# Kernel tuning notes

Measured on AMD Instinct MI355X. Metric: run time of the kernel, lower is better.

Reference implementation:

```python
import jax, jax.numpy as jnp
import numpy as np

FIR = (1.0, 3.0, 3.0, 1.0)
FACTOR = 2
GAIN = 1.0


def _fir_kernel_2d():
    # _setup_kernel: 1D -> outer product, normalize, then scale by gain*factor^2
    k = np.asarray(FIR, dtype=np.float32)
    k = np.outer(k, k)
    k /= k.sum()
    return k * (GAIN * FACTOR ** 2)  # [4, 4]


def setup_inputs() -> dict:
    key = jax.random.key(0)
    kx, kw = jax.random.split(key)
    x = jax.random.normal(kx, (4, 256, 64, 64), dtype=jnp.float32)
    # DDPM variance-scaling init ~ U(-sqrt(3*var), sqrt(3*var)); plain scaled normal is fine for a numeric baseline
    w = jax.random.normal(kw, (256, 256, 3, 3), dtype=jnp.float32) * 0.02  # [outC, inC, 3, 3]
    return {"x": x, "w": w}


def reference(x, w):
    # Fused upsample(+FIR) conv: torch does conv_transpose2d(x, flip(w).permute(in,out), stride=2)
    # which is exactly a correlation of the stride-2 zero-dilated input with the ORIGINAL OIHW weight.
    N, C, H, W = x.shape
    outC, inC, kh, kw_ = w.shape
    h = jax.lax.conv_general_dilated(
        x, w,
        window_strides=(1, 1),
        padding=((kh - 1, kh - 1), (kw_ - 1, kw_ - 1)),
        lhs_dilation=(FACTOR, FACTOR),
        dimension_numbers=("NCHW", "OIHW", "NCHW"),
    )  # [N, outC, 2H+1, 2W+1]

    k = jnp.asarray(_fir_kernel_2d())  # [4,4]
    p = k.shape[0] - FACTOR - (kw_ - 1)          # = 0
    pad0 = (p + 1) // 2 + FACTOR - 1             # = 1
    pad1 = p // 2 + 1                            # = 1
    # upfirdn2d with up=1, down=1, pad=(pad0,pad1): pad then TRUE convolution (flipped kernel),
    # applied depthwise per channel.
    kflip = k[::-1, ::-1]
    kern = jnp.tile(kflip[None, None, :, :], (outC, 1, 1, 1))  # [outC, 1, 4, 4]
    out = jax.lax.conv_general_dilated(
        h, kern,
        window_strides=(1, 1),
        padding=((pad0, pad1), (pad0, pad1)),
        dimension_numbers=("NCHW", "OIHW", "NCHW"),
        feature_group_count=outC,
    )  # [N, outC, 2H, 2W]
    return out
```

## Files before the change

### kernel.cpp

```cpp
#include <hip/hip_runtime.h>
#include <hip/hip_bf16.h>


typedef short short2v __attribute__((ext_vector_type(2)));
typedef short bf16x8 __attribute__((ext_vector_type(8)));
typedef short short4v __attribute__((ext_vector_type(4)));
typedef float f32x2v __attribute__((ext_vector_type(2)));
typedef float f32x16 __attribute__((ext_vector_type(16)));
typedef float f32x4v __attribute__((ext_vector_type(4)));

static __device__ __forceinline__ short f2bf(float f) {
  __hip_bfloat16 h = __float2bfloat16(f);
  union { __hip_bfloat16 h; short s; } u; u.h = h;
  return u.s;
}
static __device__ __forceinline__ float bf2f(short s) {
  union { unsigned u; float f; } v; v.u = ((unsigned)(unsigned short)s) << 16;
  return v.f;
}

#define AS_SZ 18432
#define XS_BASE 36864
#define XS_SZ 8640
#define XS_STRIDE 48

__global__ __launch_bounds__(512, 2)
void fir_up_v15(const float* __restrict__ x, const float* __restrict__ w,
                float* __restrict__ out) {
  __shared__ __align__(16) char smem[54144];

  const int bid = blockIdx.x;
  const int wg = (bid & 7) * 64 + (bid >> 3);
  const int octile = wg >> 7;
  const int n = (wg >> 5) & 3;
  const int sp = wg & 31;
  const int atile = sp >> 2;
  const int btile = sp & 3;
  const int A0 = atile * 8, B0 = btile * 16;

  const int tid = threadIdx.x;
  const int wid = tid >> 6;
  const int lane = tid & 63;
  const int l31 = lane & 31, q = lane >> 5;

  const int COLSt[4]  = {17, 18, 17, 18};
  const int CELLSt[4] = {153, 162, 170, 180};
  const int NKt[4]    = {4, 2, 2, 1};
  const int KQt[4][4] = {{0,2,6,8},{1,7,7,7},{3,5,5,5},{4,4,4,4}};
  const int DYt[4][4] = {{0,0,1,1},{0,1,1,1},{0,0,0,0},{0,0,0,0}};
  const int DXt[4][4] = {{0,1,0,1},{0,0,0,0},{0,1,1,1},{0,0,0,0}};
  const unsigned long long PLbits =
      (0x34ULL) | (0x34ULL << 6) | (0x34ULL << 12) | (0x38ULL << 18) |
      (0x38ULL << 24) | (0x38ULL << 30) | (0x15ULL << 36) | (0x2AULL << 42);
  const unsigned FG0 = 0u | 1u<<3 | 2u<<6 | 3u<<9 | 4u<<12 | 5u<<15 | 3u<<18 | 3u<<21;
  const unsigned FG1 = 0u | 1u<<3 | 2u<<6 | 0u<<9 | 1u<<12 | 2u<<15 | 4u<<18 | 4u<<21;
  const unsigned FG2 = 0u | 1u<<3 | 2u<<6 | 3u<<9 | 4u<<12 | 5u<<15 | 5u<<18 | 5u<<21;

  int nkS[3], validS[3], hbaseS[3];
  int kqS[3][4], cellxS[3][4];
#pragma unroll
  for (int slot = 0; slot < 3; ++slot) {
    const int p = (int)((PLbits >> ((wid * 3 + slot) * 2)) & 3ULL);
    const unsigned fgw = slot == 0 ? FG0 : (slot == 1 ? FG1 : FG2);
    const int fg = (int)((fgw >> (3 * wid)) & 7u);
    const int cellraw = fg * 32 + l31;
    const int valid = cellraw < CELLSt[p];
    const int cell = valid ? cellraw : 0;
    const int cols = COLSt[p];
    const int r = cell / cols;
    const int c = cell - r * cols;
    nkS[slot] = NKt[p];
    validS[slot] = valid;
    hbaseS[slot] = p * 6400 + r * 20 + c;
#pragma unroll
    for (int s = 0; s < 4; ++s) {
      kqS[slot][s] = KQt[p][s];
      cellxS[slot][s] = (r + DYt[p][s]) * 18 + (c + DXt[p][s]);
    }
  }

  f32x16 acc[3][2];
#pragma unroll
  for (int slot = 0; slot < 3; ++slot)
#pragma unroll
    for (int mf = 0; mf < 2; ++mf)
#pragma unroll
      for (int e = 0; e < 16; ++e) acc[slot][mf][e] = 0.f;

  const int ocA = tid >> 3, icp = tid & 7;
  const float* wA = w + (size_t)(octile * 64 + ocA) * 2304 + icp * 18;
  int uic_[2], urow_[2], uf4g_[2], ugh_[2], ugw0_[2], uwb0_[2];
  bool uact_[2], urowok_[2], ual_[2], uint_[2];
#pragma unroll
  for (int t = 0; t < 2; ++t) {
    const int u = tid + t * 512;
    uact_[t] = u < 960;
    const int uu = uact_[t] ? u : 0;
    uic_[t] = uu / 60;
    const int rem = uu - uic_[t] * 60;
    urow_[t] = rem / 6;
    uf4g_[t] = rem - urow_[t] * 6;
    ugh_[t] = A0 - 1 + urow_[t];
    urowok_[t] = (ugh_[t] >= 0) & (ugh_[t] < 64);
    ugw0_[t] = B0 - 4 + 4 * uf4g_[t];
    ual_[t] = (ugw0_[t] >= 0) & (ugw0_[t] <= 60);
    uint_[t] = (uf4g_[t] >= 1) & (uf4g_[t] <= 4);
    uwb0_[t] = (urow_[t] * 18 + (4 * uf4g_[t] - 3)) * XS_STRIDE + uic_[t] * 2;
  }

  {
    char* xsw = smem + XS_BASE;
#pragma unroll
    for (int t = 0; t < 2; ++t) {
      if (uact_[t]) {
        float v[4] = {0.f, 0.f, 0.f, 0.f};
        if (urowok_[t]) {
          const float* base = x + (((size_t)(n * 256 + uic_[t])) * 64 + ugh_[t]) * 64;
          if (ual_[t]) {
            const f32x4v fv = *(const f32x4v*)(base + ugw0_[t]);
#pragma unroll
            for (int e = 0; e < 4; ++e) v[e] = fv[e];
          } else {
#pragma unroll
            for (int e = 0; e < 4; ++e) {
              const int gw = ugw0_[t] + e;
              v[e] = (gw >= 0 && gw < 64) ? base[gw] : 0.f;
            }
          }
        }
        if (uint_[t]) {
#pragma unroll
          for (int e = 0; e < 4; ++e)
            *(short*)(xsw + uwb0_[t] + e * XS_STRIDE) = f2bf(v[e]);
        } else {
#pragma unroll
          for (int e = 0; e < 4; ++e) {
            const int ww = 4 * uf4g_[t] + e - 3;
            if (ww >= 0 && ww < 18)
              *(short*)(xsw + (urow_[t] * 18 + ww) * XS_STRIDE + uic_[t] * 2) = f2bf(v[e]);
          }
        }
      }
    }
    float f18[18];
#pragma unroll
    for (int j = 0; j < 9; ++j)
      *(f32x2v*)&f18[2 * j] = *(const f32x2v*)(wA + 2 * j);
#pragma unroll
    for (int kq = 0; kq < 9; ++kq) {
      short2v pk;
      pk[0] = f2bf(f18[kq]);
      pk[1] = f2bf(f18[kq + 9]);
      *(short2v*)(smem + kq * 2048 + ocA * 32 + icp * 4) = pk;
    }
  }
  __syncthreads();

  for (int cc = 0; cc < 16; ++cc) {
    char* Asr = smem + (cc & 1) * AS_SZ;
    char* xsr = smem + XS_BASE + (cc & 1) * XS_SZ;
    char* Asw = smem + ((cc + 1) & 1) * AS_SZ;
    char* xsw = smem + XS_BASE + ((cc + 1) & 1) * XS_SZ;
    const bool have = cc < 15;

    float xv[2][4];
#pragma unroll
    for (int t = 0; t < 2; ++t) {
#pragma unroll
      for (int e = 0; e < 4; ++e) xv[t][e] = 0.f;
      if (have && uact_[t] && urowok_[t]) {
        const float* base =
            x + (((size_t)(n * 256 + (cc + 1) * 16 + uic_[t])) * 64 + ugh_[t]) * 64;
        if (ual_[t]) {
          const f32x4v fv = *(const f32x4v*)(base + ugw0_[t]);
#pragma unroll
          for (int e = 0; e < 4; ++e) xv[t][e] = fv[e];
        } else {
#pragma unroll
          for (int e = 0; e < 4; ++e) {
            const int gw = ugw0_[t] + e;
            xv[t][e] = (gw >= 0 && gw < 64) ? base[gw] : 0.f;
          }
        }
      }
    }

    __builtin_amdgcn_s_setprio(1);
#pragma unroll
    for (int slot = 0; slot < 3; ++slot) {
#pragma unroll
      for (int s = 0; s < 4; ++s) {
        if (s < nkS[slot]) {
          const int kq = kqS[slot][s];
          const bf16x8 B  = *(const bf16x8*)(xsr + cellxS[slot][s] * XS_STRIDE + q * 16);
          const bf16x8 Aa = *(const bf16x8*)(Asr + kq * 2048 + l31 * 32 + q * 16);
          const bf16x8 Ab = *(const bf16x8*)(Asr + kq * 2048 + 1024 + l31 * 32 + q * 16);
          acc[slot][0] = __builtin_amdgcn_mfma_f32_32x32x16_bf16(Aa, B, acc[slot][0], 0, 0, 0);
          acc[slot][1] = __builtin_amdgcn_mfma_f32_32x32x16_bf16(Ab, B, acc[slot][1], 0, 0, 0);
        }
      }
    }
    __builtin_amdgcn_s_setprio(0);

    if (have) {
#pragma unroll
      for (int t = 0; t < 2; ++t) {
        if (uact_[t]) {
          if (uint_[t]) {
#pragma unroll
            for (int e = 0; e < 4; ++e)
              *(short*)(xsw + uwb0_[t] + e * XS_STRIDE) = f2bf(xv[t][e]);
          } else {
#pragma unroll
            for (int e = 0; e < 4; ++e) {
              const int ww = 4 * uf4g_[t] + e - 3;
              if (ww >= 0 && ww < 18)
                *(short*)(xsw + (urow_[t] * 18 + ww) * XS_STRIDE + uic_[t] * 2) = f2bf(xv[t][e]);
            }
          }
        }
      }
      float f18[18];
      const float* wp = wA + (cc + 1) * 144;
#pragma unroll
      for (int j = 0; j < 9; ++j)
        *(f32x2v*)&f18[2 * j] = *(const f32x2v*)(wp + 2 * j);
#pragma unroll
      for (int kq = 0; kq < 9; ++kq) {
        short2v pk;
        pk[0] = f2bf(f18[kq]);
        pk[1] = f2bf(f18[kq + 9]);
        *(short2v*)(Asw + kq * 2048 + ocA * 32 + icp * 4) = pk;
      }
    }
    __syncthreads();
  }

  short* hl = (short*)smem;
  const float kf4[4] = {0.25f, 0.75f, 0.75f, 0.25f};
#pragma unroll
  for (int mf = 0; mf < 2; ++mf) {
    if (mf) __syncthreads();
#pragma unroll
    for (int slot = 0; slot < 3; ++slot) {
      if (validS[slot]) {
#pragma unroll
        for (int e = 0; e < 16; ++e) {
          const int ocl = (e & 3) + 8 * (e >> 2) + 4 * q;
          hl[hbaseS[slot] + ocl * 200] = f2bf(acc[slot][mf][e]);
        }
      }
    }
    __syncthreads();
#pragma unroll
    for (int k = 0; k < 4; ++k) {
      const int v = tid + k * 512;
      const int g = v & 3;
      const int Yl = (v >> 2) & 15;
      const int ocl = v >> 6;
      float o[8];
#pragma unroll
      for (int xx = 0; xx < 8; ++xx) o[xx] = 0.f;
#pragma unroll
      for (int du = 0; du < 4; ++du) {
        const int ttp = Yl - 1 + du;
        const int py = ttp & 1;
        const int r = py ? ((Yl + du) >> 1) : (ttp >> 1);
        const int baseE = (py * 2) * 6400 + ocl * 200 + r * 20 + 4 * g;
        const int baseO = (py * 2 + 1) * 6400 + ocl * 200 + r * 20 + 4 * g;
        const short4v e0 = *(const short4v*)(hl + baseE);
        const short4v e1 = *(const short4v*)(hl + baseE + 4);
        const short4v o0 = *(const short4v*)(hl + baseO);
        const short4v o1 = *(const short4v*)(hl + baseO + 4);
        float E[8], O[8];
#pragma unroll
        for (int i = 0; i < 4; ++i) {
          E[i] = bf2f(e0[i]); E[i + 4] = bf2f(e1[i]);
          O[i] = bf2f(o0[i]); O[i + 4] = bf2f(o1[i]);
        }
        float rx[8];
        rx[0] = 0.25f*O[0] + 0.75f*E[0] + 0.75f*O[1] + 0.25f*E[1];
        rx[1] = 0.25f*E[0] + 0.75f*O[1] + 0.75f*E[1] + 0.25f*O[2];
        rx[2] = 0.25f*O[1] + 0.75f*E[1] + 0.75f*O[2] + 0.25f*E[2];
        rx[3] = 0.25f*E[1] + 0.75f*O[2] + 0.75f*E[2] + 0.25f*O[3];
        rx[4] = 0.25f*O[2] + 0.75f*E[2] + 0.75f*O[3] + 0.25f*E[3];
        rx[5] = 0.25f*E[2] + 0.75f*O[3] + 0.75f*E[3] + 0.25f*O[4];
        rx[6] = 0.25f*O[3] + 0.75f*E[3] + 0.75f*O[4] + 0.25f*E[4];
        rx[7] = 0.25f*E[3] + 0.75f*O[4] + 0.75f*E[4] + 0.25f*O[5];
        const float ky = kf4[du];
#pragma unroll
        for (int xx = 0; xx < 8; ++xx) o[xx] += ky * rx[xx];
      }
      const int oc = octile * 64 + mf * 32 + ocl;
      const int Y = atile * 16 + Yl;
      const int X0 = btile * 32 + g * 8;
      float* op = out + (((size_t)(n * 256 + oc)) * 128 + Y) * 128 + X0;
      f32x4v v0, v1;
      v0[0] = o[0]; v0[1] = o[1]; v0[2] = o[2]; v0[3] = o[3];
      v1[0] = o[4]; v1[1] = o[5]; v1[2] = o[6]; v1[3] = o[7];
      *(f32x4v*)op = v0;
      *(f32x4v*)(op + 4) = v1;
    }
  }
}

extern "C" void kernel_launch(void* const* d_in, const int* in_sizes, int n_in,
                              void* d_out, int out_size, void* d_ws, size_t ws_size,
                              hipStream_t stream) {
  (void)in_sizes; (void)n_in; (void)out_size; (void)d_ws; (void)ws_size;
  const float* x = (const float*)d_in[0];
  const float* w = (const float*)d_in[1];
  float* out = (float*)d_out;
  hipLaunchKernelGGL(fir_up_v15, dim3(512), dim3(512), 0, stream, x, w, out);
}
```

Baseline: 91.94 us.

## Coalesce weight loads, prefetch them before MFMAs, and XOR-swizzle the A tile in LDS

Weight tile loading now reads contiguous 16-byte float4 chunks, flattened across the oc/ic/kq layout, in place of strided 8-byte per-thread reads. The loads for the next chunk are issued before the MFMA loop, so their global latency overlaps compute. The A tile in shared memory is XOR-swizzled at 16-byte granularity, meant to cut bank conflicts on both the scattered bf16 stores and the MFMA operand reads. In exchange, each weight element is now written to LDS as a separate 2-byte store, and more registers are held for the prefetched values and precomputed offsets, which may pressure occupancy at 512 threads x 2 blocks.

```diff
diff --git a/kernel.cpp b/kernel.cpp
--- a/kernel.cpp
+++ b/kernel.cpp
@@ -2,10 +2,8 @@
 #include <hip/hip_bf16.h>
 
 
-typedef short short2v __attribute__((ext_vector_type(2)));
 typedef short bf16x8 __attribute__((ext_vector_type(8)));
 typedef short short4v __attribute__((ext_vector_type(4)));
-typedef float f32x2v __attribute__((ext_vector_type(2)));
 typedef float f32x16 __attribute__((ext_vector_type(16)));
 typedef float f32x4v __attribute__((ext_vector_type(4)));
 
@@ -18,6 +16,11 @@
   union { unsigned u; float f; } v; v.u = ((unsigned)(unsigned short)s) << 16;
   return v.f;
 }
+static __device__ __forceinline__ int swz(int off) {
+  int s = off >> 4;
+  s ^= (s >> 3) & 7;
+  return (s << 4) | (off & 15);
+}
 
 #define AS_SZ 18432
 #define XS_BASE 36864
@@ -25,7 +28,7 @@
 #define XS_STRIDE 48
 
 __global__ __launch_bounds__(512, 2)
-void fir_up_v15(const float* __restrict__ x, const float* __restrict__ w,
+void fir_up_v16(const float* __restrict__ x, const float* __restrict__ w,
                 float* __restrict__ out) {
   __shared__ __align__(16) char smem[54144];
 
@@ -79,6 +82,13 @@
     }
   }
 
+  int swzb;
+  {
+    int s = 2 * l31 + q;
+    s ^= (s >> 3) & 7;
+    swzb = s << 4;
+  }
+
   f32x16 acc[3][2];
 #pragma unroll
   for (int slot = 0; slot < 3; ++slot)
@@ -87,8 +97,27 @@
 #pragma unroll
       for (int e = 0; e < 16; ++e) acc[slot][mf][e] = 0.f;
 
-  const int ocA = tid >> 3, icp = tid & 7;
-  const float* wA = w + (size_t)(octile * 64 + ocA) * 2304 + icp * 18;
+  const char* wbase_b = (const char*)(w + (size_t)(octile * 64) * 2304);
+  int preoff[5];
+  int woff[5][4];
+  bool actA[5];
+#pragma unroll
+  for (int k = 0; k < 5; ++k) {
+    const int f = tid + k * 512;
+    actA[k] = f < 2304;
+    const int fc = actA[k] ? f : 0;
+    const int oc = fc / 36;
+    const int f36 = fc - oc * 36;
+    preoff[k] = oc * 9216 + f36 * 16;
+#pragma unroll
+    for (int e = 0; e < 4; ++e) {
+      const int flat = f36 * 4 + e;
+      const int ic = flat / 9;
+      const int kq = flat - ic * 9;
+      woff[k][e] = kq * 2048 + swz(oc * 32 + ic * 2);
+    }
+  }
+
   int uic_[2], urow_[2], uf4g_[2], ugh_[2], ugw0_[2], uwb0_[2];
   bool uact_[2], urowok_[2], ual_[2], uint_[2];
 #pragma unroll
@@ -142,16 +171,14 @@
         }
       }
     }
-    float f18[18];
-#pragma unroll
-    for (int j = 0; j < 9; ++j)
-      *(f32x2v*)&f18[2 * j] = *(const f32x2v*)(wA + 2 * j);
-#pragma unroll
-    for (int kq = 0; kq < 9; ++kq) {
-      short2v pk;
-      pk[0] = f2bf(f18[kq]);
-      pk[1] = f2bf(f18[kq + 9]);
-      *(short2v*)(smem + kq * 2048 + ocA * 32 + icp * 4) = pk;
+#pragma unroll
+    for (int k = 0; k < 5; ++k) {
+      if (actA[k]) {
+        const f32x4v v = *(const f32x4v*)(wbase_b + preoff[k]);
+#pragma unroll
+        for (int e = 0; e < 4; ++e)
+          *(short*)(smem + woff[k][e]) = f2bf(v[e]);
+      }
     }
   }
   __syncthreads();
@@ -184,6 +211,12 @@
         }
       }
     }
+    f32x4v wv[5];
+#pragma unroll
+    for (int k = 0; k < 5; ++k) {
+      if (have && actA[k])
+        wv[k] = *(const f32x4v*)(wbase_b + preoff[k] + (cc + 1) * 576);
+    }
 
     __builtin_amdgcn_s_setprio(1);
 #pragma unroll
@@ -193,8 +226,8 @@
         if (s < nkS[slot]) {
           const int kq = kqS[slot][s];
           const bf16x8 B  = *(const bf16x8*)(xsr + cellxS[slot][s] * XS_STRIDE + q * 16);
-          const bf16x8 Aa = *(const bf16x8*)(Asr + kq * 2048 + l31 * 32 + q * 16);
-          const bf16x8 Ab = *(const bf16x8*)(Asr + kq * 2048 + 1024 + l31 * 32 + q * 16);
+          const bf16x8 Aa = *(const bf16x8*)(Asr + kq * 2048 + swzb);
+          const bf16x8 Ab = *(const bf16x8*)(Asr + kq * 2048 + 1024 + swzb);
           acc[slot][0] = __builtin_amdgcn_mfma_f32_32x32x16_bf16(Aa, B, acc[slot][0], 0, 0, 0);
           acc[slot][1] = __builtin_amdgcn_mfma_f32_32x32x16_bf16(Ab, B, acc[slot][1], 0, 0, 0);
         }
@@ -220,17 +253,13 @@
           }
         }
       }
-      float f18[18];
-      const float* wp = wA + (cc + 1) * 144;
-#pragma unroll
-      for (int j = 0; j < 9; ++j)
-        *(f32x2v*)&f18[2 * j] = *(const f32x2v*)(wp + 2 * j);
-#pragma unroll
-      for (int kq = 0; kq < 9; ++kq) {
-        short2v pk;
-        pk[0] = f2bf(f18[kq]);
-        pk[1] = f2bf(f18[kq + 9]);
-        *(short2v*)(Asw + kq * 2048 + ocA * 32 + icp * 4) = pk;
+#pragma unroll
+      for (int k = 0; k < 5; ++k) {
+        if (actA[k]) {
+#pragma unroll
+          for (int e = 0; e < 4; ++e)
+            *(short*)(Asw + woff[k][e]) = f2bf(wv[k][e]);
+        }
       }
     }
     __syncthreads();
@@ -311,5 +340,5 @@
   const float* x = (const float*)d_in[0];
   const float* w = (const float*)d_in[1];
   float* out = (float*)d_out;
-  hipLaunchKernelGGL(fir_up_v15, dim3(512), dim3(512), 0, stream, x, w, out);
-}
+  hipLaunchKernelGGL(fir_up_v16, dim3(512), dim3(512), 0, stream, x, w, out);
+}
```

Result: slower. 103.5 us (+12.6%).

## Reassign wave work by phase segments to reuse weight fragments across cell groups

Applied to the files above, without the earlier changes.

Each wave now owns a contiguous segment of cell groups from a single parity phase, instead of three mixed slots. This lets it load the A (weight) fragments once per kernel tap and reuse them across up to four B fragments. Wave 2 also handles two extra phase-3 groups. The change cuts LDS reads of A and the per-slot index overhead. In exchange it needs four accumulator pairs per wave, which raises register pressure, and the load across waves may be less even.

```diff
diff --git a/kernel.cpp b/kernel.cpp
--- a/kernel.cpp
+++ b/kernel.cpp
@@ -25,7 +25,7 @@
 #define XS_STRIDE 48
 
 __global__ __launch_bounds__(512, 2)
-void fir_up_v15(const float* __restrict__ x, const float* __restrict__ w,
+void fir_up_v17(const float* __restrict__ x, const float* __restrict__ w,
                 float* __restrict__ out) {
   __shared__ __align__(16) char smem[54144];
 
@@ -49,43 +49,55 @@
   const int KQt[4][4] = {{0,2,6,8},{1,7,7,7},{3,5,5,5},{4,4,4,4}};
   const int DYt[4][4] = {{0,0,1,1},{0,1,1,1},{0,0,0,0},{0,0,0,0}};
   const int DXt[4][4] = {{0,1,0,1},{0,0,0,0},{0,1,1,1},{0,0,0,0}};
-  const unsigned long long PLbits =
-      (0x34ULL) | (0x34ULL << 6) | (0x34ULL << 12) | (0x38ULL << 18) |
-      (0x38ULL << 24) | (0x38ULL << 30) | (0x15ULL << 36) | (0x2AULL << 42);
-  const unsigned FG0 = 0u | 1u<<3 | 2u<<6 | 3u<<9 | 4u<<12 | 5u<<15 | 3u<<18 | 3u<<21;
-  const unsigned FG1 = 0u | 1u<<3 | 2u<<6 | 0u<<9 | 1u<<12 | 2u<<15 | 4u<<18 | 4u<<21;
-  const unsigned FG2 = 0u | 1u<<3 | 2u<<6 | 3u<<9 | 4u<<12 | 5u<<15 | 5u<<18 | 5u<<21;
-
-  int nkS[3], validS[3], hbaseS[3];
-  int kqS[3][4], cellxS[3][4];
-#pragma unroll
-  for (int slot = 0; slot < 3; ++slot) {
-    const int p = (int)((PLbits >> ((wid * 3 + slot) * 2)) & 3ULL);
-    const unsigned fgw = slot == 0 ? FG0 : (slot == 1 ? FG1 : FG2);
-    const int fg = (int)((fgw >> (3 * wid)) & 7u);
-    const int cellraw = fg * 32 + l31;
-    const int valid = cellraw < CELLSt[p];
+  const int SEG0P[8]   = {0,0,0,1,1,2,2,3};
+  const int SEG0FGB[8] = {0,2,4,0,3,0,3,0};
+  const int SEG0NFG[8] = {2,2,1,3,3,3,3,4};
+
+  const int p0w = SEG0P[wid];
+  const int nk0 = NKt[p0w];
+  const int nfg0 = SEG0NFG[wid];
+  int aoff0[4];
+#pragma unroll
+  for (int s = 0; s < 4; ++s)
+    aoff0[s] = KQt[p0w][s] * 2048 + l31 * 32 + q * 16;
+  int boff0[4][4], valid0[4], hbase0[4];
+#pragma unroll
+  for (int fg = 0; fg < 4; ++fg) {
+    const int cellraw = (SEG0FGB[wid] + fg) * 32 + l31;
+    const int valid = cellraw < CELLSt[p0w];
     const int cell = valid ? cellraw : 0;
-    const int cols = COLSt[p];
+    const int cols = COLSt[p0w];
     const int r = cell / cols;
     const int c = cell - r * cols;
-    nkS[slot] = NKt[p];
-    validS[slot] = valid;
-    hbaseS[slot] = p * 6400 + r * 20 + c;
+    valid0[fg] = valid;
+    hbase0[fg] = p0w * 6400 + r * 20 + c;
 #pragma unroll
     for (int s = 0; s < 4; ++s) {
-      kqS[slot][s] = KQt[p][s];
-      cellxS[slot][s] = (r + DYt[p][s]) * 18 + (c + DXt[p][s]);
-    }
-  }
-
-  f32x16 acc[3][2];
-#pragma unroll
-  for (int slot = 0; slot < 3; ++slot)
+      const int bc = (r + DYt[p0w][s]) * 18 + (c + DXt[p0w][s]);
+      boff0[fg][s] = bc * XS_STRIDE + q * 16;
+    }
+  }
+  const int aoff1 = 4 * 2048 + l31 * 32 + q * 16;
+  int boff1[2], valid1[2], hbase1[2];
+#pragma unroll
+  for (int j = 0; j < 2; ++j) {
+    const int cellraw = (4 + j) * 32 + l31;
+    const int valid = cellraw < 180;
+    const int cell = valid ? cellraw : 0;
+    const int r = cell / 18;
+    const int c = cell - r * 18;
+    valid1[j] = valid;
+    hbase1[j] = 3 * 6400 + r * 20 + c;
+    boff1[j] = cell * XS_STRIDE + q * 16;
+  }
+
+  f32x16 acc[4][2];
+#pragma unroll
+  for (int fg = 0; fg < 4; ++fg)
 #pragma unroll
     for (int mf = 0; mf < 2; ++mf)
 #pragma unroll
-      for (int e = 0; e < 16; ++e) acc[slot][mf][e] = 0.f;
+      for (int e = 0; e < 16; ++e) acc[fg][mf][e] = 0.f;
 
   const int ocA = tid >> 3, icp = tid & 7;
   const float* wA = w + (size_t)(octile * 64 + ocA) * 2304 + icp * 18;
@@ -187,17 +199,28 @@
 
     __builtin_amdgcn_s_setprio(1);
 #pragma unroll
-    for (int slot = 0; slot < 3; ++slot) {
-#pragma unroll
-      for (int s = 0; s < 4; ++s) {
-        if (s < nkS[slot]) {
-          const int kq = kqS[slot][s];
-          const bf16x8 B  = *(const bf16x8*)(xsr + cellxS[slot][s] * XS_STRIDE + q * 16);
-          const bf16x8 Aa = *(const bf16x8*)(Asr + kq * 2048 + l31 * 32 + q * 16);
-          const bf16x8 Ab = *(const bf16x8*)(Asr + kq * 2048 + 1024 + l31 * 32 + q * 16);
-          acc[slot][0] = __builtin_amdgcn_mfma_f32_32x32x16_bf16(Aa, B, acc[slot][0], 0, 0, 0);
-          acc[slot][1] = __builtin_amdgcn_mfma_f32_32x32x16_bf16(Ab, B, acc[slot][1], 0, 0, 0);
-        }
+    for (int s = 0; s < 4; ++s) {
+      if (s < nk0) {
+        const bf16x8 Aa = *(const bf16x8*)(Asr + aoff0[s]);
+        const bf16x8 Ab = *(const bf16x8*)(Asr + aoff0[s] + 1024);
+#pragma unroll
+        for (int fg = 0; fg < 4; ++fg) {
+          if (fg < nfg0) {
+            const bf16x8 B = *(const bf16x8*)(xsr + boff0[fg][s]);
+            acc[fg][0] = __builtin_amdgcn_mfma_f32_32x32x16_bf16(Aa, B, acc[fg][0], 0, 0, 0);
+            acc[fg][1] = __builtin_amdgcn_mfma_f32_32x32x16_bf16(Ab, B, acc[fg][1], 0, 0, 0);
+          }
+        }
+      }
+    }
+    if (wid == 2) {
+      const bf16x8 Aa = *(const bf16x8*)(Asr + aoff1);
+      const bf16x8 Ab = *(const bf16x8*)(Asr + aoff1 + 1024);
+#pragma unroll
+      for (int j = 0; j < 2; ++j) {
+        const bf16x8 B = *(const bf16x8*)(xsr + boff1[j]);
+        acc[1 + j][0] = __builtin_amdgcn_mfma_f32_32x32x16_bf16(Aa, B, acc[1 + j][0], 0, 0, 0);
+        acc[1 + j][1] = __builtin_amdgcn_mfma_f32_32x32x16_bf16(Ab, B, acc[1 + j][1], 0, 0, 0);
       }
     }
     __builtin_amdgcn_s_setprio(0);
@@ -242,12 +265,24 @@
   for (int mf = 0; mf < 2; ++mf) {
     if (mf) __syncthreads();
 #pragma unroll
-    for (int slot = 0; slot < 3; ++slot) {
-      if (validS[slot]) {
+    for (int fg = 0; fg < 4; ++fg) {
+      if (fg < nfg0 && valid0[fg]) {
 #pragma unroll
         for (int e = 0; e < 16; ++e) {
           const int ocl = (e & 3) + 8 * (e >> 2) + 4 * q;
-          hl[hbaseS[slot] + ocl * 200] = f2bf(acc[slot][mf][e]);
+          hl[hbase0[fg] + ocl * 200] = f2bf(acc[fg][mf][e]);
+        }
+      }
+    }
+    if (wid == 2) {
+#pragma unroll
+      for (int j = 0; j < 2; ++j) {
+        if (valid1[j]) {
+#pragma unroll
+          for (int e = 0; e < 16; ++e) {
+            const int ocl = (e & 3) + 8 * (e >> 2) + 4 * q;
+            hl[hbase1[j] + ocl * 200] = f2bf(acc[1 + j][mf][e]);
+          }
         }
       }
     }
@@ -311,5 +346,5 @@
   const float* x = (const float*)d_in[0];
   const float* w = (const float*)d_in[1];
   float* out = (float*)d_out;
-  hipLaunchKernelGGL(fir_up_v15, dim3(512), dim3(512), 0, stream, x, w, out);
+  hipLaunchKernelGGL(fir_up_v17, dim3(512), dim3(512), 0, stream, x, w, out);
 }
```

Result: faster. 85.31 us (-7.2%).
